# Optimization experiments

Measured on AMD Instinct MI355X. Metric: run time of the kernel, lower is better.

The kernel has to match this reference:

```python
import jax, jax.numpy as jnp
import numpy as np

N_HEADS = 12

def setup_inputs() -> dict:
    key = jax.random.key(0)
    ks = jax.random.split(key, 3)
    B, C, T = 4, 768, 2048
    x = jax.random.normal(ks[0], (B, C, T), dtype=jnp.float32)
    mask = jnp.ones((B, 1, 1, T), dtype=jnp.int32)  # all valid; masked_fill where mask==0
    Wqkv = jax.random.normal(ks[1], (3 * C, C), dtype=jnp.float32) * 0.02
    bqkv = jnp.zeros((3 * C,), dtype=jnp.float32)
    Wout = jax.random.normal(ks[2], (C, C), dtype=jnp.float32) * 0.02
    bout = jnp.zeros((C,), dtype=jnp.float32)
    return {"x": x, "mask": mask, "Wqkv": Wqkv, "bqkv": bqkv, "Wout": Wout, "bout": bout}


def reference(x, mask, Wqkv, bqkv, Wout, bout):
    B, C, T = x.shape
    H = N_HEADS
    d = C // H
    scale = 1.0 / jnp.sqrt(jnp.asarray(d, x.dtype))
    # 1x1 Conv1d == per-timestep matmul over channels
    qkv = jnp.einsum('oc,bct->bot', Wqkv, x) + bqkv[None, :, None]  # [B,3C,T]
    # channel dim splits as [3, H, d] per the torch view(B,3,H,d,T)
    qkv = qkv.reshape(B, 3, H, d, T).transpose(0, 1, 2, 4, 3)       # [B,3,H,T,d]
    q, k, v = qkv[:, 0], qkv[:, 1], qkv[:, 2]
    score = jnp.einsum('bhtd,bhsd->bhts', q, k) * scale             # [B,H,T,T]
    score = jnp.where(mask == 0, jnp.asarray(-10000.0, score.dtype), score)
    attn = jax.nn.softmax(score, axis=-1)  # dropout: eval mode (identity)
    o = jnp.einsum('bhts,bhsd->bhtd', attn, v)                      # [B,H,T,d]
    o = o.transpose(0, 1, 3, 2).reshape(B, C, T)                    # [B,C,T]
    return jnp.einsum('oc,bct->bot', Wout, o) + bout[None, :, None]
```

## Files before the change

kernel.cpp:

```cpp
#include <hip/hip_runtime.h>
#include <hip/hip_bf16.h>
#include <stdint.h>

#define B_   4
#define C_   768
#define T_   2048
#define H_   12
#define D_   64
#define O3_  2304

typedef __attribute__((ext_vector_type(4))) float f32x4;
typedef __attribute__((ext_vector_type(8))) short bf16x8;

__device__ __forceinline__ unsigned short f2bf(float f) {
  union { float f; unsigned int u; } v; v.f = f;
  unsigned int r = v.u + 0x7fffu + ((v.u >> 16) & 1u);
  return (unsigned short)(r >> 16);
}

__device__ __forceinline__ unsigned int pack2bf(float a, float b) {
  __hip_bfloat162 h2 = __float22bfloat162_rn(make_float2(a, b));
  union { __hip_bfloat162 h; unsigned int u; } cv; cv.h = h2;
  return cv.u;
}

__device__ __forceinline__ float fexp2(float x) {
#if __has_builtin(__builtin_amdgcn_exp2f)
  return __builtin_amdgcn_exp2f(x);
#else
  return exp2f(x);
#endif
}

__device__ __forceinline__ void async16(const void* g, void* lds) {
#if __has_builtin(__builtin_amdgcn_global_load_lds)
  __builtin_amdgcn_global_load_lds((const __attribute__((address_space(1))) void*)g,
                                   (__attribute__((address_space(3))) void*)lds, 16, 0, 0);
#else
  int lane = threadIdx.x & 63;
  *((uint4*)((char*)lds + lane * 16)) = *((const uint4*)g);
#endif
}


__global__ void cvt_f32_bf16(const float* __restrict__ in,
                             unsigned short* __restrict__ out, int n4) {
  int i = blockIdx.x * 256 + threadIdx.x;
  if (i < n4) {
    float4 f = ((const float4*)in)[i];
    ushort4 o;
    o.x = f2bf(f.x); o.y = f2bf(f.y); o.z = f2bf(f.z); o.w = f2bf(f.w);
    ((ushort4*)out)[i] = o;
  }
}

__global__ void make_bias(const int* __restrict__ mask, float* __restrict__ mbias, int n) {
  int i = blockIdx.x * 256 + threadIdx.x;
  if (i < n) mbias[i] = (mask[i] == 0) ? -14426.950408f : 0.0f;
}

__global__ void transpose_x(const float* __restrict__ x,
                            unsigned short* __restrict__ xT) {
  __shared__ unsigned short tile[32][33];
  int b = blockIdx.z;
  int c0 = blockIdx.y * 32;
  int t0 = blockIdx.x * 32;
  int tid = threadIdx.x;
  {
    int cl = tid >> 3;
    int tl = (tid & 7) * 4;
    float4 f = *(const float4*)(x + ((size_t)b * C_ + c0 + cl) * T_ + t0 + tl);
    tile[tl + 0][cl] = f2bf(f.x);
    tile[tl + 1][cl] = f2bf(f.y);
    tile[tl + 2][cl] = f2bf(f.z);
    tile[tl + 3][cl] = f2bf(f.w);
  }
  __syncthreads();
  {
    int tl = tid >> 3;
    int cl = (tid & 7) * 4;
    ushort4 o;
    o.x = tile[tl][cl + 0]; o.y = tile[tl][cl + 1];
    o.z = tile[tl][cl + 2]; o.w = tile[tl][cl + 3];
    *(ushort4*)(xT + ((size_t)b * T_ + t0 + tl) * C_ + c0 + cl) = o;
  }
}

__global__ __launch_bounds__(256, 3)
void gemm_qkv(const unsigned short* __restrict__ xT,
              const unsigned short* __restrict__ W1,
              const float* __restrict__ bqkv,
              unsigned short* __restrict__ Qb,
              unsigned short* __restrict__ Kb,
              unsigned short* __restrict__ Vb) {
  __shared__ unsigned short sA[3][128 * 32];
  __shared__ unsigned short sB[3][128 * 32];

  const int b   = blockIdx.z;
  const int o0  = blockIdx.y * 128;
  const int t0  = blockIdx.x * 128;
  const int tid = threadIdx.x;
  const int wave = tid >> 6, lane = tid & 63;
  const int q = lane >> 4, ln = lane & 15;
  const int tw = wave >> 1, ow = wave & 1;

  {
    const int lin = blockIdx.x + 16 * (blockIdx.y + 18 * blockIdx.z);
    const int ph = lin >> 8;
    if (ph == 1) __builtin_amdgcn_s_sleep(5);
    else if (ph == 2) __builtin_amdgcn_s_sleep(10);
  }

  const unsigned short* Ax = xT + (size_t)b * T_ * C_;
  const int srow = lane >> 2;
  const int ssw  = ((lane >> 2) ^ (lane >> 4)) & 3;
  const int scol = ((lane & 3) ^ ssw) * 8;
  const int rsw  = (ln ^ (ln >> 2)) & 3;

  const f32x4 ZERO = {0.f, 0.f, 0.f, 0.f};
  f32x4 acc[4][4];
#pragma unroll
  for (int mi = 0; mi < 4; ++mi)
#pragma unroll
    for (int ni = 0; ni < 4; ++ni) acc[mi][ni] = ZERO;

  auto stageA = [&](int ks, int bufi) {
#pragma unroll
    for (int j = 0; j < 2; ++j) {
      const int chunk = wave * 2 + j;
      async16(Ax + (size_t)(t0 + chunk * 16 + srow) * C_ + ks * 32 + scol,
              &sA[bufi][chunk * 512]);
    }
  };
  auto stageB = [&](int ks, int bufi) {
#pragma unroll
    for (int j = 0; j < 2; ++j) {
      const int chunk = wave * 2 + j;
      async16(W1 + (size_t)(o0 + chunk * 16 + srow) * C_ + ks * 32 + scol,
              &sB[bufi][chunk * 512]);
    }
  };
  auto sync4 = [&]() {
    __builtin_amdgcn_sched_barrier(0);
    asm volatile("s_waitcnt vmcnt(4) lgkmcnt(0)" ::: "memory");
    __builtin_amdgcn_s_barrier();
    __builtin_amdgcn_sched_barrier(0);
  };
  auto sync0 = [&]() {
    __builtin_amdgcn_sched_barrier(0);
    asm volatile("s_waitcnt vmcnt(0) lgkmcnt(0)" ::: "memory");
    __builtin_amdgcn_s_barrier();
    __builtin_amdgcn_sched_barrier(0);
  };
  auto compute = [&](int bufi) {
    bf16x8 aF[4], bF[4];
#pragma unroll
    for (int mi = 0; mi < 4; ++mi)
      aF[mi] = *(const bf16x8*)(&sA[bufi][(tw * 64 + mi * 16 + ln) * 32 + ((q ^ rsw) << 3)]);
#pragma unroll
    for (int ni = 0; ni < 4; ++ni)
      bF[ni] = *(const bf16x8*)(&sB[bufi][(ow * 64 + ni * 16 + ln) * 32 + ((q ^ rsw) << 3)]);
#pragma unroll
    for (int mi = 0; mi < 4; ++mi)
#pragma unroll
      for (int ni = 0; ni < 4; ++ni)
        acc[mi][ni] = __builtin_amdgcn_mfma_f32_16x16x32_bf16(aF[mi], bF[ni], acc[mi][ni], 0, 0, 0);
  };

  stageA(0, 0); stageB(0, 0);
  stageA(1, 1); stageB(1, 1);

  for (int g = 0; g < 7; ++g) {
    const int t3 = g * 3;
    sync4(); stageA(t3 + 2, 2); stageB(t3 + 2, 2); compute(0);
    sync4(); stageA(t3 + 3, 0); stageB(t3 + 3, 0); compute(1);
    sync4(); stageA(t3 + 4, 1); stageB(t3 + 4, 1); compute(2);
  }
  sync4(); stageA(23, 2); stageB(23, 2); compute(0);
  sync4(); compute(1);
  sync0(); compute(2);

  const float QSCL = 0.125f * 1.44269504f;
#pragma unroll
  for (int ni = 0; ni < 4; ++ni) {
    const int o = o0 + ow * 64 + ni * 16 + ln;
    const float bias = bqkv[o];
    const int which = o / C_;
    const int rem = o - which * C_;
    const int bh = b * H_ + (rem >> 6);
    const int dd = rem & 63;
#pragma unroll
    for (int mi = 0; mi < 4; ++mi) {
      const int tb = t0 + tw * 64 + mi * 16 + q * 4;
      f32x4 v = acc[mi][ni];
      if (which == 0) {
#pragma unroll
        for (int r = 0; r < 4; ++r)
          Qb[((size_t)bh * T_ + tb + r) * D_ + dd] = f2bf((v[r] + bias) * QSCL);
      } else if (which == 1) {
#pragma unroll
        for (int r = 0; r < 4; ++r) {
          const int s = tb + r;
          const int cp = (dd >> 3) ^ (s & 7);
          Kb[((size_t)bh * T_ + s) * 64 + (cp << 3) + (dd & 7)] = f2bf(v[r] + bias);
        }
      } else {
        const int tile = tb >> 6, si = tb & 63;
        const int cp = (si >> 3) ^ (dd & 7);
        ushort4 pk;
        pk.x = f2bf(v[0] + bias);
        pk.y = f2bf(v[1] + bias);
        pk.z = f2bf(v[2] + bias);
        pk.w = f2bf(v[3] + bias);
        *(ushort4*)(Vb + (((size_t)bh * 32 + tile) * 64 + dd) * 64 + (cp << 3) + (si & 7)) = pk;
      }
    }
  }
}

__global__ __launch_bounds__(256, 3)
void attn(const unsigned short* __restrict__ Qb,
          const unsigned short* __restrict__ Kb,
          const unsigned short* __restrict__ Vb,
          const float* __restrict__ mbias,
          unsigned short* __restrict__ Ob) {
  __shared__ __align__(16) char smem[49152];
  unsigned short* sK0 = (unsigned short*)smem;
  unsigned short* sV0 = (unsigned short*)(smem + 24576);

  const int id = blockIdx.x;
  const int bh = id % 48;
  const int tblk = id / 48;
  const int b = bh / H_, h = bh % H_;
  const int tid = threadIdx.x, wave = tid >> 6, lane = tid & 63;
  const int q = lane >> 4, ln = lane & 15;
  const int t0w = tblk * 128 + wave * 32;

  {
    const int ph = id >> 8;
    if (ph == 1) __builtin_amdgcn_s_sleep(9);
    else if (ph == 2) __builtin_amdgcn_s_sleep(18);
  }

  bf16x8 Qa[2][2];
#pragma unroll
  for (int tt = 0; tt < 2; ++tt) {
    const unsigned short* qrow = Qb + ((size_t)bh * T_ + t0w + tt * 16 + ln) * D_;
    Qa[tt][0] = *(const bf16x8*)(qrow + q * 8);
    Qa[tt][1] = *(const bf16x8*)(qrow + 32 + q * 8);
  }

  const f32x4 ZERO = {0.f, 0.f, 0.f, 0.f};
  f32x4 Oacc[4][2];
  f32x4 lacc[2];
#pragma unroll
  for (int dt = 0; dt < 4; ++dt)
#pragma unroll
    for (int tt = 0; tt < 2; ++tt) Oacc[dt][tt] = ZERO;
#pragma unroll
  for (int tt = 0; tt < 2; ++tt) lacc[tt] = ZERO;

  const short one_s = (ln == 0) ? (short)0x3F80 : (short)0;
  bf16x8 ones;
#pragma unroll
  for (int j = 0; j < 8; ++j) ones[j] = one_s;

  const unsigned short* gK = Kb + (size_t)bh * T_ * 64;
  const unsigned short* gV = Vb + (size_t)bh * 32 * 4096;
  const float* mb = mbias + b * T_;

  unsigned int maskbits = 0;
  for (int t2 = 0; t2 < 32; ++t2)
    if (__ballot(mb[t2 * 64 + lane] != 0.0f) != 0ull) maskbits |= (1u << t2);

  auto stage = [&](const unsigned short* g, unsigned short* lds) {
#pragma unroll
    for (int j = 0; j < 2; ++j) {
      const int chunk = wave * 2 + j;
      async16(g + chunk * 512 + lane * 8, lds + chunk * 512);
    }
  };

  auto sync4 = [&]() {
    __builtin_amdgcn_sched_barrier(0);
    asm volatile("s_waitcnt vmcnt(4) lgkmcnt(0)" ::: "memory");
    __builtin_amdgcn_s_barrier();
    __builtin_amdgcn_sched_barrier(0);
  };
  auto sync0 = [&]() {
    __builtin_amdgcn_sched_barrier(0);
    asm volatile("s_waitcnt vmcnt(0) lgkmcnt(0)" ::: "memory");
    __builtin_amdgcn_s_barrier();
    __builtin_amdgcn_sched_barrier(0);
  };

  auto QK = [&](const unsigned short* sKc, int it, bf16x8 pfO[2][2]) {
    const int s0 = it * 64;
    const bool anymask = (maskbits >> it) & 1;
#pragma unroll
    for (int kc = 0; kc < 2; ++kc) {
      bf16x8 kf0[2], kf1[2];
#pragma unroll
      for (int sb = 0; sb < 2; ++sb) {
        const unsigned short* krow = sKc + (kc * 32 + sb * 16 + ln) * 64;
        kf0[sb] = *(const bf16x8*)(krow + ((q ^ (ln & 7)) << 3));
        kf1[sb] = *(const bf16x8*)(krow + (((4 + q) ^ (ln & 7)) << 3));
      }
#pragma unroll
      for (int tt = 0; tt < 2; ++tt) {
        f32x4 sc[2];
        __builtin_amdgcn_s_setprio(1);
#pragma unroll
        for (int sb = 0; sb < 2; ++sb) {
          f32x4 p0 = __builtin_amdgcn_mfma_f32_16x16x32_bf16(kf0[sb], Qa[tt][0], ZERO, 0, 0, 0);
          sc[sb]   = __builtin_amdgcn_mfma_f32_16x16x32_bf16(kf1[sb], Qa[tt][1], p0, 0, 0, 0);
        }
        __builtin_amdgcn_s_setprio(0);
        if (anymask) {
#pragma unroll
          for (int sb = 0; sb < 2; ++sb) {
            f32x4 bb = *(const f32x4*)(mb + s0 + kc * 32 + sb * 16 + q * 4);
#pragma unroll
            for (int r = 0; r < 4; ++r) sc[sb][r] += bb[r];
          }
        }
        unsigned int A0 = pack2bf(fexp2(sc[0][0]), fexp2(sc[0][1]));
        unsigned int B0 = pack2bf(fexp2(sc[0][2]), fexp2(sc[0][3]));
        unsigned int C0 = pack2bf(fexp2(sc[1][0]), fexp2(sc[1][1]));
        unsigned int E0 = pack2bf(fexp2(sc[1][2]), fexp2(sc[1][3]));
        asm volatile("v_permlane32_swap_b32 %0, %1" : "+v"(A0), "+v"(C0));
        asm volatile("v_permlane16_swap_b32 %0, %1" : "+v"(A0), "+v"(C0));
        asm volatile("v_permlane32_swap_b32 %0, %1" : "+v"(B0), "+v"(E0));
        asm volatile("v_permlane16_swap_b32 %0, %1" : "+v"(B0), "+v"(E0));
        union { bf16x8 v; unsigned int u[4]; } P;
        P.u[0] = A0;
        P.u[1] = B0;
        P.u[2] = C0;
        P.u[3] = E0;
        pfO[tt][kc] = P.v;
      }
    }
  };

  auto PV = [&](const unsigned short* sVc, bf16x8 pfI[2][2]) {
    __builtin_amdgcn_s_setprio(1);
#pragma unroll
    for (int dt = 0; dt < 4; ++dt) {
#pragma unroll
      for (int kc = 0; kc < 2; ++kc) {
        bf16x8 vf = *(const bf16x8*)(sVc + (dt * 16 + ln) * 64 +
                                     (((kc * 4 + q) ^ (ln & 7)) << 3));
#pragma unroll
        for (int tt = 0; tt < 2; ++tt)
          Oacc[dt][tt] = __builtin_amdgcn_mfma_f32_16x16x32_bf16(vf, pfI[tt][kc], Oacc[dt][tt], 0, 0, 0);
      }
    }
#pragma unroll
    for (int kc = 0; kc < 2; ++kc)
#pragma unroll
      for (int tt = 0; tt < 2; ++tt)
        lacc[tt] = __builtin_amdgcn_mfma_f32_16x16x32_bf16(ones, pfI[tt][kc], lacc[tt], 0, 0, 0);
    __builtin_amdgcn_s_setprio(0);
  };

  bf16x8 pf[2][2];

  stage(gK, sK0);
  stage(gV, sV0);
  stage(gK + 4096, sK0 + 4096);
  stage(gV + 4096, sV0 + 4096);

  for (int ith = 0; ith < 10; ++ith) {
    const int it = ith * 3;
    sync4();
    stage(gK + (size_t)(it + 2) * 4096, sK0 + 2 * 4096);
    stage(gV + (size_t)(it + 2) * 4096, sV0 + 2 * 4096);
    QK(sK0, it, pf);
    PV(sV0, pf);
    sync4();
    stage(gK + (size_t)(it + 3) * 4096, sK0);
    stage(gV + (size_t)(it + 3) * 4096, sV0);
    QK(sK0 + 4096, it + 1, pf);
    PV(sV0 + 4096, pf);
    sync4();
    stage(gK + (size_t)(it + 4) * 4096, sK0 + 4096);
    stage(gV + (size_t)(it + 4) * 4096, sV0 + 4096);
    QK(sK0 + 2 * 4096, it + 2, pf);
    PV(sV0 + 2 * 4096, pf);
  }

  sync4();
  QK(sK0, 30, pf);
  PV(sV0, pf);
  sync0();
  QK(sK0 + 4096, 31, pf);
  PV(sV0 + 4096, pf);

#pragma unroll
  for (int tt = 0; tt < 2; ++tt) {
    const float lv = __shfl(lacc[tt][0], ln, 64);
    const float inv = 1.0f / lv;
    const int t = t0w + tt * 16 + ln;
#pragma unroll
    for (int dt = 0; dt < 4; ++dt) {
      f32x4 o = Oacc[dt][tt];
      ushort4 pk;
      pk.x = f2bf(o[0] * inv);
      pk.y = f2bf(o[1] * inv);
      pk.z = f2bf(o[2] * inv);
      pk.w = f2bf(o[3] * inv);
      *(ushort4*)(Ob + ((size_t)b * T_ + t) * C_ + h * D_ + dt * 16 + q * 4) = pk;
    }
  }
}

__global__ __launch_bounds__(256, 3)
void gemm_out(const unsigned short* __restrict__ Ob,
              const unsigned short* __restrict__ W2,
              const float* __restrict__ bout,
              float* __restrict__ out) {
  __shared__ unsigned short sA[3][64 * 32];
  __shared__ unsigned short sB[3][128 * 32];

  const int b   = blockIdx.z;
  const int o0  = blockIdx.y * 64;
  const int t0  = blockIdx.x * 128;
  const int tid = threadIdx.x;
  const int wave = tid >> 6, lane = tid & 63;
  const int q = lane >> 4, ln = lane & 15;
  const int tw = wave >> 1, ow = wave & 1;

  {
    const int lin = blockIdx.x + 16 * (blockIdx.y + 12 * blockIdx.z);
    const int ph = lin >> 8;
    if (ph == 1) __builtin_amdgcn_s_sleep(5);
    else if (ph == 2) __builtin_amdgcn_s_sleep(10);
  }

  const unsigned short* Bo = Ob + (size_t)b * T_ * C_;
  const int srow = lane >> 2;
  const int ssw  = ((lane >> 2) ^ (lane >> 4)) & 3;
  const int scol = ((lane & 3) ^ ssw) * 8;
  const int rsw  = (ln ^ (ln >> 2)) & 3;

  const f32x4 ZERO = {0.f, 0.f, 0.f, 0.f};
  f32x4 acc[2][4];
#pragma unroll
  for (int mi = 0; mi < 2; ++mi)
#pragma unroll
    for (int ni = 0; ni < 4; ++ni) acc[mi][ni] = ZERO;

  auto stageA = [&](int ks, int bufi) {
    async16(W2 + (size_t)(o0 + wave * 16 + srow) * C_ + ks * 32 + scol,
            &sA[bufi][wave * 512]);
  };
  auto stageB = [&](int ks, int bufi) {
#pragma unroll
    for (int j = 0; j < 2; ++j) {
      const int chunk = wave * 2 + j;
      async16(Bo + (size_t)(t0 + chunk * 16 + srow) * C_ + ks * 32 + scol,
              &sB[bufi][chunk * 512]);
    }
  };
  auto sync3 = [&]() {
    __builtin_amdgcn_sched_barrier(0);
    asm volatile("s_waitcnt vmcnt(3) lgkmcnt(0)" ::: "memory");
    __builtin_amdgcn_s_barrier();
    __builtin_amdgcn_sched_barrier(0);
  };
  auto sync0 = [&]() {
    __builtin_amdgcn_sched_barrier(0);
    asm volatile("s_waitcnt vmcnt(0) lgkmcnt(0)" ::: "memory");
    __builtin_amdgcn_s_barrier();
    __builtin_amdgcn_sched_barrier(0);
  };
  auto compute = [&](int bufi) {
    bf16x8 aF[2], bF[4];
#pragma unroll
    for (int mi = 0; mi < 2; ++mi)
      aF[mi] = *(const bf16x8*)(&sA[bufi][(tw * 32 + mi * 16 + ln) * 32 + ((q ^ rsw) << 3)]);
#pragma unroll
    for (int ni = 0; ni < 4; ++ni)
      bF[ni] = *(const bf16x8*)(&sB[bufi][(ow * 64 + ni * 16 + ln) * 32 + ((q ^ rsw) << 3)]);
#pragma unroll
    for (int mi = 0; mi < 2; ++mi)
#pragma unroll
      for (int ni = 0; ni < 4; ++ni)
        acc[mi][ni] = __builtin_amdgcn_mfma_f32_16x16x32_bf16(aF[mi], bF[ni], acc[mi][ni], 0, 0, 0);
  };

  stageA(0, 0); stageB(0, 0);
  stageA(1, 1); stageB(1, 1);

  for (int g = 0; g < 7; ++g) {
    const int t3 = g * 3;
    sync3(); stageA(t3 + 2, 2); stageB(t3 + 2, 2); compute(0);
    sync3(); stageA(t3 + 3, 0); stageB(t3 + 3, 0); compute(1);
    sync3(); stageA(t3 + 4, 1); stageB(t3 + 4, 1); compute(2);
  }
  sync3(); stageA(23, 2); stageB(23, 2); compute(0);
  sync3(); compute(1);
  sync0(); compute(2);

#pragma unroll
  for (int mi = 0; mi < 2; ++mi) {
    const int ob = o0 + tw * 32 + mi * 16 + q * 4;
#pragma unroll
    for (int ni = 0; ni < 4; ++ni) {
      const int t = t0 + ow * 64 + ni * 16 + ln;
      f32x4 v = acc[mi][ni];
#pragma unroll
      for (int r = 0; r < 4; ++r)
        out[((size_t)b * C_ + ob + r) * T_ + t] = v[r] + bout[ob + r];
    }
  }
}


extern "C" void kernel_launch(void* const* d_in, const int* in_sizes, int n_in,
                              void* d_out, int out_size, void* d_ws, size_t ws_size,
                              hipStream_t stream) {
  (void)in_sizes; (void)n_in; (void)out_size; (void)ws_size;
  const float* x    = (const float*)d_in[0];
  const int*   mask = (const int*)d_in[1];
  const float* Wqkv = (const float*)d_in[2];
  const float* bqkv = (const float*)d_in[3];
  const float* Wout = (const float*)d_in[4];
  const float* bout = (const float*)d_in[5];
  float* out = (float*)d_out;

  const size_t szHead = (size_t)B_ * H_ * T_ * D_;
  const size_t szBTC  = (size_t)B_ * T_ * C_;
  unsigned short* Qb  = (unsigned short*)d_ws;
  unsigned short* Kb  = Qb + szHead;
  unsigned short* Vb  = Kb + szHead;
  unsigned short* Ob  = Vb + szHead;
  unsigned short* xT  = Ob + szBTC;
  unsigned short* W1b = xT + szBTC;
  unsigned short* W2b = W1b + (size_t)O3_ * C_;
  float* mbias        = (float*)(W2b + (size_t)C_ * C_);

  cvt_f32_bf16<<<dim3((O3_ * C_ / 4 + 255) / 256), 256, 0, stream>>>(Wqkv, W1b, O3_ * C_ / 4);
  cvt_f32_bf16<<<dim3((C_ * C_ / 4 + 255) / 256), 256, 0, stream>>>(Wout, W2b, C_ * C_ / 4);
  make_bias<<<dim3((B_ * T_ + 255) / 256), 256, 0, stream>>>(mask, mbias, B_ * T_);
  transpose_x<<<dim3(T_ / 32, C_ / 32, B_), 256, 0, stream>>>(x, xT);
  gemm_qkv<<<dim3(T_ / 128, O3_ / 128, B_), 256, 0, stream>>>(xT, W1b, bqkv, Qb, Kb, Vb);
  attn<<<dim3(768), 256, 0, stream>>>(Qb, Kb, Vb, mbias, Ob);
  gemm_out<<<dim3(T_ / 128, C_ / 64, B_), 256, 0, stream>>>(Ob, W2b, bout, out);
}
```

Measured before the change: 225.7 us.

## Restage QKV GEMM with four-buffer pipeline, LDS-staged epilogue, drop sleeps and setprio

The QKV GEMM moves from a three-buffer, one-step-ahead pipeline to four LDS buffers that load two k-steps at a time with full waits. Its scattered per-element Q/K/V stores now go through LDS and leave as coalesced 16-byte writes. Separately, the staggered s_sleep launch delays are removed from all three kernels, and the setprio hints and mask-add placement change in attention. The larger LDS footprint lowers the occupancy bound to 2 blocks, and the full vmcnt(0) waits may expose more load latency.

After: 230.1 us. No clear change (+1.9%).

```diff
diff --git a/kernel.cpp b/kernel.cpp
--- a/kernel.cpp
+++ b/kernel.cpp
@@ -86,15 +86,15 @@
   }
 }
 
-__global__ __launch_bounds__(256, 3)
+__global__ __launch_bounds__(256, 2)
 void gemm_qkv(const unsigned short* __restrict__ xT,
               const unsigned short* __restrict__ W1,
               const float* __restrict__ bqkv,
               unsigned short* __restrict__ Qb,
               unsigned short* __restrict__ Kb,
               unsigned short* __restrict__ Vb) {
-  __shared__ unsigned short sA[3][128 * 32];
-  __shared__ unsigned short sB[3][128 * 32];
+  __shared__ unsigned short sA[4][128 * 32];
+  __shared__ unsigned short sB[4][128 * 32];
 
   const int b   = blockIdx.z;
   const int o0  = blockIdx.y * 128;
@@ -104,13 +104,6 @@
   const int q = lane >> 4, ln = lane & 15;
   const int tw = wave >> 1, ow = wave & 1;
 
-  {
-    const int lin = blockIdx.x + 16 * (blockIdx.y + 18 * blockIdx.z);
-    const int ph = lin >> 8;
-    if (ph == 1) __builtin_amdgcn_s_sleep(5);
-    else if (ph == 2) __builtin_amdgcn_s_sleep(10);
-  }
-
   const unsigned short* Ax = xT + (size_t)b * T_ * C_;
   const int srow = lane >> 2;
   const int ssw  = ((lane >> 2) ^ (lane >> 4)) & 3;
@@ -140,12 +133,6 @@
               &sB[bufi][chunk * 512]);
     }
   };
-  auto sync4 = [&]() {
-    __builtin_amdgcn_sched_barrier(0);
-    asm volatile("s_waitcnt vmcnt(4) lgkmcnt(0)" ::: "memory");
-    __builtin_amdgcn_s_barrier();
-    __builtin_amdgcn_sched_barrier(0);
-  };
   auto sync0 = [&]() {
     __builtin_amdgcn_sched_barrier(0);
     asm volatile("s_waitcnt vmcnt(0) lgkmcnt(0)" ::: "memory");
@@ -170,51 +157,76 @@
   stageA(0, 0); stageB(0, 0);
   stageA(1, 1); stageB(1, 1);
 
-  for (int g = 0; g < 7; ++g) {
-    const int t3 = g * 3;
-    sync4(); stageA(t3 + 2, 2); stageB(t3 + 2, 2); compute(0);
-    sync4(); stageA(t3 + 3, 0); stageB(t3 + 3, 0); compute(1);
-    sync4(); stageA(t3 + 4, 1); stageB(t3 + 4, 1); compute(2);
-  }
-  sync4(); stageA(23, 2); stageB(23, 2); compute(0);
-  sync4(); compute(1);
-  sync0(); compute(2);
-
+  for (int p = 0; p < 5; ++p) {
+    const int t4 = p * 4;
+    sync0();
+    stageA(t4 + 2, 2); stageB(t4 + 2, 2);
+    stageA(t4 + 3, 3); stageB(t4 + 3, 3);
+    compute(0); compute(1);
+    sync0();
+    stageA(t4 + 4, 0); stageB(t4 + 4, 0);
+    stageA(t4 + 5, 1); stageB(t4 + 5, 1);
+    compute(2); compute(3);
+  }
+  sync0();
+  stageA(22, 2); stageB(22, 2);
+  stageA(23, 3); stageB(23, 3);
+  compute(0); compute(1);
+  sync0();
+  compute(2); compute(3);
+
+  __syncthreads();
+  unsigned short* eb = &sA[0][0];
   const float QSCL = 0.125f * 1.44269504f;
+  const int whichB = o0 / C_;
 #pragma unroll
   for (int ni = 0; ni < 4; ++ni) {
     const int o = o0 + ow * 64 + ni * 16 + ln;
     const float bias = bqkv[o];
-    const int which = o / C_;
-    const int rem = o - which * C_;
-    const int bh = b * H_ + (rem >> 6);
-    const int dd = rem & 63;
+    const int dd = ni * 16 + ln;
 #pragma unroll
     for (int mi = 0; mi < 4; ++mi) {
       const int tb = t0 + tw * 64 + mi * 16 + q * 4;
+      const int tl128 = tb - t0;
       f32x4 v = acc[mi][ni];
-      if (which == 0) {
+      if (whichB == 0) {
 #pragma unroll
         for (int r = 0; r < 4; ++r)
-          Qb[((size_t)bh * T_ + tb + r) * D_ + dd] = f2bf((v[r] + bias) * QSCL);
-      } else if (which == 1) {
+          eb[ow * 8192 + (tl128 + r) * 64 + dd] = f2bf((v[r] + bias) * QSCL);
+      } else if (whichB == 1) {
 #pragma unroll
         for (int r = 0; r < 4; ++r) {
           const int s = tb + r;
           const int cp = (dd >> 3) ^ (s & 7);
-          Kb[((size_t)bh * T_ + s) * 64 + (cp << 3) + (dd & 7)] = f2bf(v[r] + bias);
+          eb[ow * 8192 + (tl128 + r) * 64 + (cp << 3) + (dd & 7)] = f2bf(v[r] + bias);
         }
       } else {
-        const int tile = tb >> 6, si = tb & 63;
+        const int tl = tl128 >> 6;
+        const int si = tb & 63;
         const int cp = (si >> 3) ^ (dd & 7);
         ushort4 pk;
         pk.x = f2bf(v[0] + bias);
         pk.y = f2bf(v[1] + bias);
         pk.z = f2bf(v[2] + bias);
         pk.w = f2bf(v[3] + bias);
-        *(ushort4*)(Vb + (((size_t)bh * 32 + tile) * 64 + dd) * 64 + (cp << 3) + (si & 7)) = pk;
+        *(ushort4*)(eb + ow * 8192 + tl * 4096 + dd * 64 + (cp << 3) + (si & 7)) = pk;
       }
     }
+  }
+  __syncthreads();
+  {
+    const int remB = o0 - whichB * C_;
+    const int bh0 = b * H_ + (remB >> 6);
+    const int hl = wave >> 1, hf = wave & 1;
+    unsigned short* gdst;
+    if (whichB == 0)      gdst = Qb + ((size_t)(bh0 + hl) * T_ + t0) * D_;
+    else if (whichB == 1) gdst = Kb + ((size_t)(bh0 + hl) * T_ + t0) * 64;
+    else                  gdst = Vb + ((size_t)(bh0 + hl) * 32 + (t0 >> 6)) * 4096;
+    gdst += hf * 4096;
+    const unsigned short* src = eb + hl * 8192 + hf * 4096;
+#pragma unroll
+    for (int k = 0; k < 8; ++k)
+      *(uint4*)(gdst + k * 512 + lane * 8) = *(const uint4*)(src + k * 512 + lane * 8);
   }
 }
 
@@ -236,12 +248,6 @@
   const int q = lane >> 4, ln = lane & 15;
   const int t0w = tblk * 128 + wave * 32;
 
-  {
-    const int ph = id >> 8;
-    if (ph == 1) __builtin_amdgcn_s_sleep(9);
-    else if (ph == 2) __builtin_amdgcn_s_sleep(18);
-  }
-
   bf16x8 Qa[2][2];
 #pragma unroll
   for (int tt = 0; tt < 2; ++tt) {
@@ -309,16 +315,11 @@
 #pragma unroll
       for (int tt = 0; tt < 2; ++tt) {
         f32x4 sc[2];
-        __builtin_amdgcn_s_setprio(1);
 #pragma unroll
         for (int sb = 0; sb < 2; ++sb) {
           f32x4 p0 = __builtin_amdgcn_mfma_f32_16x16x32_bf16(kf0[sb], Qa[tt][0], ZERO, 0, 0, 0);
           sc[sb]   = __builtin_amdgcn_mfma_f32_16x16x32_bf16(kf1[sb], Qa[tt][1], p0, 0, 0, 0);
-        }
-        __builtin_amdgcn_s_setprio(0);
-        if (anymask) {
-#pragma unroll
-          for (int sb = 0; sb < 2; ++sb) {
+          if (anymask) {
             f32x4 bb = *(const f32x4*)(mb + s0 + kc * 32 + sb * 16 + q * 4);
 #pragma unroll
             for (int r = 0; r < 4; ++r) sc[sb][r] += bb[r];
@@ -343,7 +344,6 @@
   };
 
   auto PV = [&](const unsigned short* sVc, bf16x8 pfI[2][2]) {
-    __builtin_amdgcn_s_setprio(1);
 #pragma unroll
     for (int dt = 0; dt < 4; ++dt) {
 #pragma unroll
@@ -360,7 +360,6 @@
 #pragma unroll
       for (int tt = 0; tt < 2; ++tt)
         lacc[tt] = __builtin_amdgcn_mfma_f32_16x16x32_bf16(ones, pfI[tt][kc], lacc[tt], 0, 0, 0);
-    __builtin_amdgcn_s_setprio(0);
   };
 
   bf16x8 pf[2][2];
@@ -430,13 +429,6 @@
   const int q = lane >> 4, ln = lane & 15;
   const int tw = wave >> 1, ow = wave & 1;
 
-  {
-    const int lin = blockIdx.x + 16 * (blockIdx.y + 12 * blockIdx.z);
-    const int ph = lin >> 8;
-    if (ph == 1) __builtin_amdgcn_s_sleep(5);
-    else if (ph == 2) __builtin_amdgcn_s_sleep(10);
-  }
-
   const unsigned short* Bo = Ob + (size_t)b * T_ * C_;
   const int srow = lane >> 2;
   const int ssw  = ((lane >> 2) ^ (lane >> 4)) & 3;
```
